# Kernel optimization log

Measured on AMD Instinct MI355X. Metric: run time of the kernel, lower is better.

## Reference

```python
import jax, jax.numpy as jnp
import numpy as np

C = 512        # in_ch = n_heads * d_embed
NH = 8         # heads
DH = C // NH   # head dim = 64
G = 32         # groups
EPS_GN = 1e-6
EPS_LN = 1e-5


def group_norm(x, gamma, beta):
    # x: (B, C, H, W)
    B, Cc, H, W = x.shape
    xg = x.reshape(B, G, Cc // G, H, W)
    mu = xg.mean(axis=(2, 3, 4), keepdims=True)
    var = xg.var(axis=(2, 3, 4), keepdims=True)
    xg = (xg - mu) * jax.lax.rsqrt(var + EPS_GN)
    x = xg.reshape(B, Cc, H, W)
    return x * gamma[None, :, None, None] + beta[None, :, None, None]


def layer_norm(x, gamma, beta):
    mu = x.mean(axis=-1, keepdims=True)
    var = x.var(axis=-1, keepdims=True)
    return (x - mu) * jax.lax.rsqrt(var + EPS_LN) * gamma + beta


def mhsa(x, w_qkv, w_out, b_out):
    # x: (B, S, C); w_qkv: (C, 3C); w_out: (C, C)
    B, S, Cc = x.shape
    qkv = x @ w_qkv                                   # (B, S, 3C)
    q, k, v = jnp.split(qkv, 3, axis=-1)
    q = q.reshape(B, S, NH, DH).transpose(0, 2, 1, 3)  # (B, H, S, D)
    k = k.reshape(B, S, NH, DH).transpose(0, 2, 1, 3)
    v = v.reshape(B, S, NH, DH).transpose(0, 2, 1, 3)
    scores = jnp.einsum('bhsd,bhtd->bhst', q, k) / jnp.sqrt(jnp.float32(DH))
    attn = jax.nn.softmax(scores, axis=-1)
    o = jnp.einsum('bhst,bhtd->bhsd', attn, v)         # (B, H, S, D)
    o = o.transpose(0, 2, 1, 3).reshape(B, S, Cc)
    return o @ w_out + b_out


def conv1x1(x, w, b):
    # x: (B, C, H, W); w: (Cout, Cin)
    return jnp.einsum('oc,bchw->bohw', w, x) + b[None, :, None, None]


def reference(x, gn_g, gn_b, w_cin, b_cin,
              ln1_g, ln1_b, qkv1, out1_w, out1_b,
              ln2_g, ln2_b, qkv2, out2_w, out2_b,
              ln3_g, ln3_b, g1_w, g1_b, g2_w, g2_b,
              w_cout, b_cout):
    residue_long = x
    h = group_norm(x, gn_g, gn_b)
    h = conv1x1(h, w_cin, b_cin)
    B, Cc, H, W = h.shape
    h = h.reshape(B, Cc, H * W).transpose(0, 2, 1)     # (B, S, C)

    r = h
    h = mhsa(layer_norm(h, ln1_g, ln1_b), qkv1, out1_w, out1_b) + r
    r = h
    h = mhsa(layer_norm(h, ln2_g, ln2_b), qkv2, out2_w, out2_b) + r
    r = h
    g = layer_norm(h, ln3_g, ln3_b) @ g1_w + g1_b      # (B, S, 8C)
    val, gate = jnp.split(g, 2, axis=-1)
    h = (val * jax.nn.gelu(gate, approximate=False)) @ g2_w + g2_b
    h = h + r

    h = h.transpose(0, 2, 1).reshape(B, Cc, H, W)
    return conv1x1(h, w_cout, b_cout) + residue_long


def setup_inputs() -> dict:
    key = jax.random.key(0)
    ks = jax.random.split(key, 16)
    s = lambda n: 1.0 / np.sqrt(n)
    return {
        'x': jax.random.normal(ks[0], (8, C, 32, 32), jnp.float32),
        'gn_g': jnp.ones((C,), jnp.float32),
        'gn_b': jnp.zeros((C,), jnp.float32),
        'w_cin': jax.random.normal(ks[1], (C, C), jnp.float32) * s(C),
        'b_cin': jnp.zeros((C,), jnp.float32),
        'ln1_g': jnp.ones((C,), jnp.float32),
        'ln1_b': jnp.zeros((C,), jnp.float32),
        'qkv1': jax.random.normal(ks[2], (C, 3 * C), jnp.float32) * s(C),
        'out1_w': jax.random.normal(ks[3], (C, C), jnp.float32) * s(C),
        'out1_b': jnp.zeros((C,), jnp.float32),
        'ln2_g': jnp.ones((C,), jnp.float32),
        'ln2_b': jnp.zeros((C,), jnp.float32),
        'qkv2': jax.random.normal(ks[4], (C, 3 * C), jnp.float32) * s(C),
        'out2_w': jax.random.normal(ks[5], (C, C), jnp.float32) * s(C),
        'out2_b': jnp.zeros((C,), jnp.float32),
        'ln3_g': jnp.ones((C,), jnp.float32),
        'ln3_b': jnp.zeros((C,), jnp.float32),
        'g1_w': jax.random.normal(ks[6], (C, 8 * C), jnp.float32) * s(C),
        'g1_b': jnp.zeros((8 * C,), jnp.float32),
        'g2_w': jax.random.normal(ks[7], (4 * C, C), jnp.float32) * s(4 * C),
        'g2_b': jnp.zeros((C,), jnp.float32),
        'w_cout': jax.random.normal(ks[8], (C, C), jnp.float32) * s(C),
        'b_cout': jnp.zeros((C,), jnp.float32),
    }
```

## Files before the change

kernel.cpp:

```cpp
#include <hip/hip_runtime.h>
#include <hip/hip_bf16.h>
#include <math.h>

typedef __hip_bfloat16 bf16;

typedef __bf16 bf16x8 __attribute__((ext_vector_type(8)));
typedef float f32x4 __attribute__((ext_vector_type(4)));
typedef short shortx8 __attribute__((ext_vector_type(8)));

__device__ __forceinline__ float b2f_us(unsigned short u) {
    unsigned int v = ((unsigned int)u) << 16;
    return __builtin_bit_cast(float, v);
}
__device__ __forceinline__ unsigned short f2b_us(float f) {
    return __builtin_bit_cast(unsigned short, __float2bfloat16(f));
}
__device__ __forceinline__ float4 ld4(const float* p) { return *(const float4*)p; }
__device__ __forceinline__ float4 ld4(const bf16* p) {
    ushort4 u = *(const ushort4*)p;
    return make_float4(b2f_us(u.x), b2f_us(u.y), b2f_us(u.z), b2f_us(u.w));
}
__device__ __forceinline__ bf16x8 ldfrag(const bf16* p) {
    return __builtin_bit_cast(bf16x8, *(const shortx8*)p);
}
__device__ __forceinline__ f32x4 mfma16(bf16x8 a, bf16x8 b, f32x4 c) {
    return __builtin_amdgcn_mfma_f32_16x16x32_bf16(a, b, c, 0, 0, 0);
}
__device__ __forceinline__ void gload16(const bf16* g, bf16* l) {
    __builtin_amdgcn_global_load_lds(
        (const __attribute__((address_space(1))) void*)g,
        (__attribute__((address_space(3))) void*)l, 16, 0, 0);
}

struct WJob { const float* src; bf16* dst; int R, C, tile0, trans; };
struct WJobs { WJob j[8]; };

__global__ __launch_bounds__(256) void wconv_all(WJobs jobs) {
    __shared__ float tl[32][33];
    int bid = blockIdx.x;
    int ji = 0;
#pragma unroll
    for (int i = 1; i < 8; ++i)
        if (bid >= jobs.j[i].tile0) ji = i;
    WJob jb = jobs.j[ji];
    int t = bid - jb.tile0;
    int tc = jb.C >> 5;
    int tr_ = t / tc, tcx = t - tr_ * tc;
    int r0 = tr_ * 32, c0 = tcx * 32;
    const int tx = threadIdx.x & 31, ty = threadIdx.x >> 5;
    if (jb.trans) {
#pragma unroll
        for (int i = 0; i < 4; ++i)
            tl[ty + i * 8][tx] = jb.src[(long)(r0 + ty + i * 8) * jb.C + c0 + tx];
        __syncthreads();
#pragma unroll
        for (int i = 0; i < 4; ++i)
            jb.dst[(long)(c0 + ty + i * 8) * jb.R + r0 + tx] =
                __float2bfloat16(tl[tx][ty + i * 8]);
    } else {
#pragma unroll
        for (int i = 0; i < 4; ++i) {
            long idx = (long)(r0 + ty + i * 8) * jb.C + c0 + tx;
            jb.dst[idx] = __float2bfloat16(jb.src[idx]);
        }
    }
}

__global__ __launch_bounds__(256) void gn_stats_k(const float* __restrict__ x,
                                                  float* __restrict__ stats) {
    int bg = blockIdx.x;
    long base = (long)bg * 16384;
    int tid = threadIdx.x;
    float s = 0.f, sq = 0.f;
    for (int it = 0; it < 16; ++it) {
        float4 v = *(const float4*)(x + base + (long)it * 1024 + tid * 4);
        s += v.x + v.y + v.z + v.w;
        sq += v.x * v.x + v.y * v.y + v.z * v.z + v.w * v.w;
    }
#pragma unroll
    for (int off = 32; off; off >>= 1) {
        s += __shfl_down(s, off);
        sq += __shfl_down(sq, off);
    }
    __shared__ float r0[4], r1[4];
    if ((tid & 63) == 0) { r0[tid >> 6] = s; r1[tid >> 6] = sq; }
    __syncthreads();
    if (tid == 0) {
        s = r0[0] + r0[1] + r0[2] + r0[3];
        sq = r1[0] + r1[1] + r1[2] + r1[3];
        float mu = s * (1.f / 16384.f);
        float var = sq * (1.f / 16384.f) - mu * mu;
        stats[bg] = mu;
        stats[256 + bg] = rsqrtf(var + 1e-6f);
    }
}

__global__ __launch_bounds__(256) void gnxt_k(const float* __restrict__ x,
                                              const float* __restrict__ stats,
                                              const float* __restrict__ gng,
                                              const float* __restrict__ gnb,
                                              bf16* __restrict__ xt) {
    const int b = blockIdx.z;
    const int c0 = blockIdx.y * 64, s0 = blockIdx.x * 64;
    __shared__ float t[64][65];
    const int tx = threadIdx.x & 15, ty = threadIdx.x >> 4;
#pragma unroll
    for (int i = 0; i < 4; ++i) {
        int c = c0 + ty + i * 16;
        float rs = stats[256 + b * 32 + (c >> 4)];
        float ga = gng[c] * rs;
        float be = gnb[c] - stats[b * 32 + (c >> 4)] * ga;
        float4 v = *(const float4*)(x + ((long)b * 512 + c) * 1024 + s0 + tx * 4);
        t[ty + i * 16][tx * 4 + 0] = v.x * ga + be;
        t[ty + i * 16][tx * 4 + 1] = v.y * ga + be;
        t[ty + i * 16][tx * 4 + 2] = v.z * ga + be;
        t[ty + i * 16][tx * 4 + 3] = v.w * ga + be;
    }
    __syncthreads();
#pragma unroll
    for (int i = 0; i < 4; ++i) {
        int s = s0 + ty + i * 16;
        ushort4 o;
        o.x = f2b_us(t[tx * 4 + 0][ty + i * 16]);
        o.y = f2b_us(t[tx * 4 + 1][ty + i * 16]);
        o.z = f2b_us(t[tx * 4 + 2][ty + i * 16]);
        o.w = f2b_us(t[tx * 4 + 3][ty + i * 16]);
        *(ushort4*)(xt + ((long)b * 1024 + s) * 512 + c0 + tx * 4) = o;
    }
}

__global__ __launch_bounds__(256) void ln_k(const bf16* __restrict__ in,
                                            const float* __restrict__ g,
                                            const float* __restrict__ bvec,
                                            bf16* __restrict__ out) {
    long row = blockIdx.x;
    const bf16* p = in + row * 512;
    int tid = threadIdx.x;
    float v0 = b2f_us(__builtin_bit_cast(unsigned short, p[tid]));
    float v1 = b2f_us(__builtin_bit_cast(unsigned short, p[tid + 256]));
    float s = v0 + v1, sq = v0 * v0 + v1 * v1;
#pragma unroll
    for (int off = 32; off; off >>= 1) {
        s += __shfl_down(s, off);
        sq += __shfl_down(sq, off);
    }
    __shared__ float r0[4], r1[4];
    if ((tid & 63) == 0) { r0[tid >> 6] = s; r1[tid >> 6] = sq; }
    __syncthreads();
    s = r0[0] + r0[1] + r0[2] + r0[3];
    sq = r1[0] + r1[1] + r1[2] + r1[3];
    float mu = s * (1.f / 512.f);
    float var = sq * (1.f / 512.f) - mu * mu;
    float rs = rsqrtf(var + 1e-5f);
    out[row * 512 + tid] = __float2bfloat16((v0 - mu) * rs * g[tid] + bvec[tid]);
    out[row * 512 + tid + 256] =
        __float2bfloat16((v1 - mu) * rs * g[tid + 256] + bvec[tid + 256]);
}

template <bool HASBIAS, bool HASRES>
__global__ __launch_bounds__(256, 2) void mm_k(
    const bf16* __restrict__ A, const bf16* __restrict__ Bw,
    const float* __restrict__ bias, const bf16* __restrict__ res,
    bf16* __restrict__ C, int lda, int ldb, int ldc, int NT) {
    __shared__ bf16 sA[8192];
    __shared__ bf16 sB[8192];
    const int lane = threadIdx.x & 63, wave = threadIdx.x >> 6;
    const int lr = lane & 15, lg = lane >> 4;
    const int wm = wave >> 1, wn = wave & 1;
    const int m0 = blockIdx.y * 128, n0 = blockIdx.x * 128;

    f32x4 acc[4][4];
#pragma unroll
    for (int i = 0; i < 4; ++i)
#pragma unroll
        for (int j = 0; j < 4; ++j) acc[i][j] = (f32x4){0.f, 0.f, 0.f, 0.f};

    for (int t = 0; t < NT; ++t) {
        const int k0 = t * 64;
#pragma unroll
        for (int q = 0; q < 4; ++q) {
            int st = wave * 4 + q;
            int kh = st >> 3, sm = st & 7;
            gload16(A + (long)(m0 + sm * 16 + lr) * lda + k0 + kh * 32 + lg * 8,
                    &sA[st << 9]);
            gload16(Bw + (long)(n0 + sm * 16 + lr) * ldb + k0 + kh * 32 + lg * 8,
                    &sB[st << 9]);
        }
        asm volatile("s_waitcnt vmcnt(0) lgkmcnt(0)" ::: "memory");
        __builtin_amdgcn_s_barrier();
#pragma unroll
        for (int kh = 0; kh < 2; ++kh) {
            bf16x8 af[4], bfr[4];
#pragma unroll
            for (int i = 0; i < 4; ++i)
                af[i] = ldfrag(&sA[((kh * 8 + wm * 4 + i) << 9) + lane * 8]);
#pragma unroll
            for (int j = 0; j < 4; ++j)
                bfr[j] = ldfrag(&sB[((kh * 8 + wn * 4 + j) << 9) + lane * 8]);
#pragma unroll
            for (int i = 0; i < 4; ++i)
#pragma unroll
                for (int j = 0; j < 4; ++j)
                    acc[i][j] = mfma16(af[i], bfr[j], acc[i][j]);
        }
        __builtin_amdgcn_s_barrier();
    }

#pragma unroll
    for (int i = 0; i < 4; ++i) {
        int row = m0 + wm * 64 + i * 16 + lg * 4;
#pragma unroll
        for (int j = 0; j < 4; ++j) {
            int col = n0 + wn * 64 + j * 16 + lr;
            float bv = HASBIAS ? bias[col] : 0.f;
#pragma unroll
            for (int r = 0; r < 4; ++r) {
                float v = acc[i][j][r] + bv;
                if (HASRES)
                    v += b2f_us(__builtin_bit_cast(unsigned short,
                             res[(long)(row + r) * ldc + col]));
                C[(long)(row + r) * ldc + col] = __float2bfloat16(v);
            }
        }
    }
}

__global__ __launch_bounds__(256, 2) void mm_geglu_k(
    const bf16* __restrict__ A, const bf16* __restrict__ Bv,
    const bf16* __restrict__ Bg, const float* __restrict__ bias,
    bf16* __restrict__ C, int NT) {
    __shared__ bf16 sA[8192];
    __shared__ bf16 sB[8192];
    const int lane = threadIdx.x & 63, wave = threadIdx.x >> 6;
    const int lr = lane & 15, lg = lane >> 4;
    const int wm = wave >> 1, wn = wave & 1;
    const int m0 = blockIdx.y * 128, n0 = blockIdx.x * 64;

    f32x4 accv[4][2], accg[4][2];
#pragma unroll
    for (int i = 0; i < 4; ++i)
#pragma unroll
        for (int j = 0; j < 2; ++j) {
            accv[i][j] = (f32x4){0.f, 0.f, 0.f, 0.f};
            accg[i][j] = (f32x4){0.f, 0.f, 0.f, 0.f};
        }

    for (int t = 0; t < NT; ++t) {
        const int k0 = t * 64;
#pragma unroll
        for (int q = 0; q < 4; ++q) {
            int st = wave * 4 + q;
            int kh = st >> 3, sm = st & 7;
            gload16(A + (long)(m0 + sm * 16 + lr) * 512 + k0 + kh * 32 + lg * 8,
                    &sA[st << 9]);
            const bf16* bsrc = (sm < 4) ? Bv : Bg;
            int sn = sm & 3;
            gload16(bsrc + (long)(n0 + sn * 16 + lr) * 512 + k0 + kh * 32 + lg * 8,
                    &sB[st << 9]);
        }
        asm volatile("s_waitcnt vmcnt(0) lgkmcnt(0)" ::: "memory");
        __builtin_amdgcn_s_barrier();
#pragma unroll
        for (int kh = 0; kh < 2; ++kh) {
            bf16x8 af[4], bv_[2], bg_[2];
#pragma unroll
            for (int i = 0; i < 4; ++i)
                af[i] = ldfrag(&sA[((kh * 8 + wm * 4 + i) << 9) + lane * 8]);
#pragma unroll
            for (int j = 0; j < 2; ++j) {
                bv_[j] = ldfrag(&sB[((kh * 8 + wn * 2 + j) << 9) + lane * 8]);
                bg_[j] = ldfrag(&sB[((kh * 8 + 4 + wn * 2 + j) << 9) + lane * 8]);
            }
#pragma unroll
            for (int i = 0; i < 4; ++i)
#pragma unroll
                for (int j = 0; j < 2; ++j) {
                    accv[i][j] = mfma16(af[i], bv_[j], accv[i][j]);
                    accg[i][j] = mfma16(af[i], bg_[j], accg[i][j]);
                }
        }
        __builtin_amdgcn_s_barrier();
    }

#pragma unroll
    for (int i = 0; i < 4; ++i) {
        int row = m0 + wm * 64 + i * 16 + lg * 4;
#pragma unroll
        for (int j = 0; j < 2; ++j) {
            int col = n0 + (wn * 2 + j) * 16 + lr;
            float bv = bias[col], bg2 = bias[2048 + col];
#pragma unroll
            for (int r = 0; r < 4; ++r) {
                float v = accv[i][j][r] + bv;
                float g = accg[i][j][r] + bg2;
                float gl = 0.5f * g * (1.f + erff(g * 0.70710678118654752f));
                C[(long)(row + r) * 2048 + col] = __float2bfloat16(v * gl);
            }
        }
    }
}

__global__ __launch_bounds__(256) void vtrans_k(const bf16* __restrict__ qkv,
                                                bf16* __restrict__ vt) {
    const int bh = blockIdx.y;
    const int b = bh >> 3, h = bh & 7;
    const int s0 = blockIdx.x * 64;
    __shared__ bf16 tl[64][72];
    const int sl = threadIdx.x >> 2, q = threadIdx.x & 3;
    const bf16* src = qkv + ((long)b * 1024 + s0 + sl) * 1536 + 1024 + h * 64;
    *(shortx8*)&tl[sl][q * 8] = *(const shortx8*)(src + q * 8);
    *(shortx8*)&tl[sl][32 + q * 8] = *(const shortx8*)(src + 32 + q * 8);
    __syncthreads();
    const int dl = threadIdx.x >> 2;
    bf16* dst = vt + ((long)bh * 64 + dl) * 1024 + s0;
#pragma unroll
    for (int c = 0; c < 2; ++c) {
        int sb = c * 32 + q * 8;
        shortx8 o;
#pragma unroll
        for (int i = 0; i < 8; ++i)
            o[i] = __builtin_bit_cast(short, tl[sb + i][dl]);
        *(shortx8*)(dst + sb) = o;
    }
}

__global__ __launch_bounds__(256) void attn_mfma_k(const bf16* __restrict__ qkv,
                                                   const bf16* __restrict__ vt,
                                                   bf16* __restrict__ o) {
    const int wave = threadIdx.x >> 6, lane = threadIdx.x & 63;
    const int lr = lane & 15, lg = lane >> 4;
    const int h = blockIdx.y, b = blockIdx.z;
    const int q0 = blockIdx.x * 128 + wave * 32;
    __shared__ bf16 sKV[8192];
    __shared__ bf16 plds[4][16][72];
    bf16* pl = &plds[wave][0][0];
    const bf16* qbase = qkv + (long)b * 1024 * 1536 + h * 64;
    const bf16* kbase = qbase + 512;
    const bf16* vbase = vt + ((long)(b * 8 + h) * 64) * 1024;

    bf16x8 qf[2][2];
#pragma unroll
    for (int s = 0; s < 2; ++s) {
        const bf16* qp = qbase + (long)(q0 + s * 16 + lr) * 1536 + lg * 8;
#pragma unroll
        for (int c = 0; c < 2; ++c) {
            shortx8 raw = *(const shortx8*)(qp + c * 32);
            shortx8 sc;
#pragma unroll
            for (int j = 0; j < 8; ++j)
                sc[j] = __builtin_bit_cast(short,
                    f2b_us(b2f_us((unsigned short)raw[j]) * 0.125f));
            qf[s][c] = __builtin_bit_cast(bf16x8, sc);
        }
    }

    f32x4 of[2][4];
    float mrow[2][4], lrow[2][4];
#pragma unroll
    for (int s = 0; s < 2; ++s)
#pragma unroll
        for (int r = 0; r < 4; ++r) {
            of[s][r] = (f32x4){0.f, 0.f, 0.f, 0.f};
            mrow[s][r] = -1e30f;
            lrow[s][r] = 0.f;
        }

    for (int t = 0; t < 16; ++t) {
        const int kv0 = t * 64;
#pragma unroll
        for (int q = 0; q < 4; ++q) {
            int st = wave * 4 + q;
            const bf16* src;
            if (st < 8)
                src = kbase + (long)(kv0 + (st >> 1) * 16 + lr) * 1536 +
                      (st & 1) * 32 + lg * 8;
            else
                src = vbase + (long)(((st - 8) >> 1) * 16 + lr) * 1024 + kv0 +
                      (st & 1) * 32 + lg * 8;
            gload16(src, &sKV[st << 9]);
        }
        asm volatile("s_waitcnt vmcnt(0) lgkmcnt(0)" ::: "memory");
        __builtin_amdgcn_s_barrier();

        f32x4 sf[2][4];
        __builtin_amdgcn_s_setprio(1);
#pragma unroll
        for (int kt = 0; kt < 4; ++kt) {
            bf16x8 k0f = ldfrag(&sKV[(kt * 2) * 512 + lane * 8]);
            bf16x8 k1f = ldfrag(&sKV[(kt * 2 + 1) * 512 + lane * 8]);
#pragma unroll
            for (int s = 0; s < 2; ++s) {
                f32x4 z = {0.f, 0.f, 0.f, 0.f};
                z = mfma16(qf[s][0], k0f, z);
                z = mfma16(qf[s][1], k1f, z);
                sf[s][kt] = z;
            }
        }
        __builtin_amdgcn_s_setprio(0);

        bf16x8 pa[2][2];
#pragma unroll
        for (int s = 0; s < 2; ++s) {
            float mt[4];
#pragma unroll
            for (int r = 0; r < 4; ++r)
                mt[r] = fmaxf(fmaxf(sf[s][0][r], sf[s][1][r]),
                              fmaxf(sf[s][2][r], sf[s][3][r]));
#pragma unroll
            for (int m = 1; m < 16; m <<= 1)
#pragma unroll
                for (int r = 0; r < 4; ++r)
                    mt[r] = fmaxf(mt[r], __shfl_xor(mt[r], m));
            float al[4];
#pragma unroll
            for (int r = 0; r < 4; ++r) {
                float mn = fmaxf(mrow[s][r], mt[r]);
                al[r] = __expf(mrow[s][r] - mn);
                mrow[s][r] = mn;
            }
            float psum[4] = {0.f, 0.f, 0.f, 0.f};
#pragma unroll
            for (int kt = 0; kt < 4; ++kt)
#pragma unroll
                for (int r = 0; r < 4; ++r) {
                    float p = __expf(sf[s][kt][r] - mrow[s][r]);
                    psum[r] += p;
                    pl[(lg * 4 + r) * 72 + kt * 16 + lr] = __float2bfloat16(p);
                }
#pragma unroll
            for (int m = 1; m < 16; m <<= 1)
#pragma unroll
                for (int r = 0; r < 4; ++r)
                    psum[r] += __shfl_xor(psum[r], m);
#pragma unroll
            for (int r = 0; r < 4; ++r)
                lrow[s][r] = lrow[s][r] * al[r] + psum[r];
#pragma unroll
            for (int dt = 0; dt < 4; ++dt)
#pragma unroll
                for (int r = 0; r < 4; ++r) of[s][dt][r] *= al[r];
            pa[s][0] = ldfrag(pl + lr * 72 + lg * 8);
            pa[s][1] = ldfrag(pl + lr * 72 + 32 + lg * 8);
        }
        __builtin_amdgcn_s_setprio(1);
#pragma unroll
        for (int dt = 0; dt < 4; ++dt) {
            bf16x8 v0f = ldfrag(&sKV[(8 + dt * 2) * 512 + lane * 8]);
            bf16x8 v1f = ldfrag(&sKV[(8 + dt * 2 + 1) * 512 + lane * 8]);
#pragma unroll
            for (int s = 0; s < 2; ++s) {
                of[s][dt] = mfma16(pa[s][0], v0f, of[s][dt]);
                of[s][dt] = mfma16(pa[s][1], v1f, of[s][dt]);
            }
        }
        __builtin_amdgcn_s_setprio(0);
        __builtin_amdgcn_s_barrier();
    }

#pragma unroll
    for (int s = 0; s < 2; ++s) {
        bf16* op = o + ((long)b * 1024 + q0 + s * 16 + lg * 4) * 512 + h * 64 + lr;
#pragma unroll
        for (int r = 0; r < 4; ++r) {
            float inv = 1.f / lrow[s][r];
#pragma unroll
            for (int dt = 0; dt < 4; ++dt)
                op[(long)r * 512 + dt * 16] = __float2bfloat16(of[s][dt][r] * inv);
        }
    }
}

__global__ __launch_bounds__(256) void outepi_k(const bf16* __restrict__ tmp,
                                                const float* __restrict__ bcout,
                                                const float* __restrict__ x,
                                                float* __restrict__ out) {
    const int b = blockIdx.z;
    const int o0 = blockIdx.y * 64, s0 = blockIdx.x * 64;
    __shared__ float t[64][65];
    const int tx = threadIdx.x & 15, ty = threadIdx.x >> 4;
#pragma unroll
    for (int i = 0; i < 4; ++i) {
        int s = s0 + ty + i * 16;
        float4 v = ld4(tmp + ((long)b * 1024 + s) * 512 + o0 + tx * 4);
        t[ty + i * 16][tx * 4 + 0] = v.x;
        t[ty + i * 16][tx * 4 + 1] = v.y;
        t[ty + i * 16][tx * 4 + 2] = v.z;
        t[ty + i * 16][tx * 4 + 3] = v.w;
    }
    __syncthreads();
#pragma unroll
    for (int i = 0; i < 4; ++i) {
        int o = o0 + ty + i * 16;
        long idx = ((long)b * 512 + o) * 1024 + s0 + tx * 4;
        float4 xr = *(const float4*)(x + idx);
        float bc = bcout[o];
        float4 w;
        w.x = t[tx * 4 + 0][ty + i * 16] + bc + xr.x;
        w.y = t[tx * 4 + 1][ty + i * 16] + bc + xr.y;
        w.z = t[tx * 4 + 2][ty + i * 16] + bc + xr.z;
        w.w = t[tx * 4 + 3][ty + i * 16] + bc + xr.w;
        *(float4*)(out + idx) = w;
    }
}

extern "C" void kernel_launch(void* const* d_in, const int* in_sizes, int n_in,
                              void* d_out, int out_size, void* d_ws, size_t ws_size,
                              hipStream_t stream) {
    const float* x = (const float*)d_in[0];
    const float* gn_g = (const float*)d_in[1];
    const float* gn_b = (const float*)d_in[2];
    const float* w_cin = (const float*)d_in[3];
    const float* b_cin = (const float*)d_in[4];
    const float* ln1_g = (const float*)d_in[5];
    const float* ln1_b = (const float*)d_in[6];
    const float* qkv1w = (const float*)d_in[7];
    const float* out1_w = (const float*)d_in[8];
    const float* out1_b = (const float*)d_in[9];
    const float* ln2_g = (const float*)d_in[10];
    const float* ln2_b = (const float*)d_in[11];
    const float* qkv2w = (const float*)d_in[12];
    const float* out2_w = (const float*)d_in[13];
    const float* out2_b = (const float*)d_in[14];
    const float* ln3_g = (const float*)d_in[15];
    const float* ln3_b = (const float*)d_in[16];
    const float* g1_w = (const float*)d_in[17];
    const float* g1_b = (const float*)d_in[18];
    const float* g2_w = (const float*)d_in[19];
    const float* g2_b = (const float*)d_in[20];
    const float* w_cout = (const float*)d_in[21];
    const float* b_cout = (const float*)d_in[22];
    float* out = (float*)d_out;

    char* ws = (char*)d_ws;
    float* stats = (float*)ws;
    bf16* wq1 = (bf16*)(ws + 4096);
    bf16* wo1 = wq1 + 1536 * 512;
    bf16* wq2 = wo1 + 512 * 512;
    bf16* wo2 = wq2 + 1536 * 512;
    bf16* wg1 = wo2 + 512 * 512;
    bf16* wg2 = wg1 + 4096 * 512;
    bf16* wci = wg2 + 512 * 2048;
    bf16* wco = wci + 512 * 512;
    bf16* h = wco + 512 * 512;
    bf16* h2 = h + (size_t)8192 * 512;
    bf16* lnb = h2 + (size_t)8192 * 512;
    bf16* qkv = lnb + (size_t)8192 * 512;
    bf16* obuf = qkv + (size_t)8192 * 1536;
    bf16* gg = qkv;
    bf16* vt = lnb;

    WJobs jobs;
    jobs.j[0] = {qkv1w, wq1, 512, 1536, 0, 1};
    jobs.j[1] = {out1_w, wo1, 512, 512, 768, 1};
    jobs.j[2] = {qkv2w, wq2, 512, 1536, 1024, 1};
    jobs.j[3] = {out2_w, wo2, 512, 512, 1792, 1};
    jobs.j[4] = {g1_w, wg1, 512, 4096, 2048, 1};
    jobs.j[5] = {g2_w, wg2, 2048, 512, 4096, 1};
    jobs.j[6] = {w_cin, wci, 512, 512, 5120, 0};
    jobs.j[7] = {w_cout, wco, 512, 512, 5376, 0};
    wconv_all<<<5632, 256, 0, stream>>>(jobs);

    gn_stats_k<<<256, 256, 0, stream>>>(x, stats);
    gnxt_k<<<dim3(16, 8, 8), 256, 0, stream>>>(x, stats, gn_g, gn_b, lnb);
    mm_k<true, false><<<dim3(4, 64), 256, 0, stream>>>(
        lnb, wci, b_cin, nullptr, h, 512, 512, 512, 8);

    ln_k<<<8192, 256, 0, stream>>>(h, ln1_g, ln1_b, lnb);
    mm_k<false, false><<<dim3(12, 64), 256, 0, stream>>>(
        lnb, wq1, nullptr, nullptr, qkv, 512, 512, 1536, 8);
    vtrans_k<<<dim3(16, 64), 256, 0, stream>>>(qkv, vt);
    attn_mfma_k<<<dim3(8, 8, 8), 256, 0, stream>>>(qkv, vt, obuf);
    mm_k<true, true><<<dim3(4, 64), 256, 0, stream>>>(
        obuf, wo1, out1_b, h, h2, 512, 512, 512, 8);

    ln_k<<<8192, 256, 0, stream>>>(h2, ln2_g, ln2_b, lnb);
    mm_k<false, false><<<dim3(12, 64), 256, 0, stream>>>(
        lnb, wq2, nullptr, nullptr, qkv, 512, 512, 1536, 8);
    vtrans_k<<<dim3(16, 64), 256, 0, stream>>>(qkv, vt);
    attn_mfma_k<<<dim3(8, 8, 8), 256, 0, stream>>>(qkv, vt, obuf);
    mm_k<true, true><<<dim3(4, 64), 256, 0, stream>>>(
        obuf, wo2, out2_b, h2, h, 512, 512, 512, 8);

    ln_k<<<8192, 256, 0, stream>>>(h, ln3_g, ln3_b, lnb);
    mm_geglu_k<<<dim3(32, 64), 256, 0, stream>>>(
        lnb, wg1, wg1 + (size_t)2048 * 512, g1_b, gg, 8);
    mm_k<true, true><<<dim3(4, 64), 256, 0, stream>>>(
        gg, wg2, g2_b, h, h2, 2048, 2048, 512, 32);

    mm_k<false, false><<<dim3(4, 64), 256, 0, stream>>>(
        h2, wco, nullptr, nullptr, lnb, 512, 512, 512, 8);
    outepi_k<<<dim3(16, 8, 8), 256, 0, stream>>>(lnb, b_cout, x, out);
}
```

Measured before the change: 436.2 us.

## Narrow GEMM tiles for N=512, fuse V transpose into QKV GEMM, lazy softmax rescale

Templates the GEMM on tile width, so the N=512 GEMMs use 128x64 tiles with twice the blocks, and raises launch bounds to 3 blocks per CU. The QKV GEMM epilogue writes V directly in transposed layout, which removes the separate vtrans kernel and its extra pass over memory. Attention now loads 128 keys per barrier instead of 64, and skips the online-softmax rescale unless the running max grows by more than 8. Each of these changes costs something: smaller tiles reuse less data, LDS usage grows, and the lazy rescale bounds exponents only by e^8 before normalisation.

```diff
diff --git a/kernel.cpp b/kernel.cpp
--- a/kernel.cpp
+++ b/kernel.cpp
@@ -157,23 +157,25 @@
         __float2bfloat16((v1 - mu) * rs * g[tid + 256] + bvec[tid + 256]);
 }
 
-template <bool HASBIAS, bool HASRES>
-__global__ __launch_bounds__(256, 2) void mm_k(
+template <bool HASBIAS, bool HASRES, int BN, bool VSPLIT>
+__global__ __launch_bounds__(256, 3) void mm_k(
     const bf16* __restrict__ A, const bf16* __restrict__ Bw,
     const float* __restrict__ bias, const bf16* __restrict__ res,
-    bf16* __restrict__ C, int lda, int ldb, int ldc, int NT) {
+    bf16* __restrict__ C, bf16* __restrict__ vtout,
+    int lda, int ldb, int ldc, int NT) {
+    constexpr int NJ = BN / 64 * 2;
     __shared__ bf16 sA[8192];
-    __shared__ bf16 sB[8192];
+    __shared__ bf16 sB[BN == 128 ? 8192 : 4096];
     const int lane = threadIdx.x & 63, wave = threadIdx.x >> 6;
     const int lr = lane & 15, lg = lane >> 4;
     const int wm = wave >> 1, wn = wave & 1;
-    const int m0 = blockIdx.y * 128, n0 = blockIdx.x * 128;
-
-    f32x4 acc[4][4];
+    const int m0 = blockIdx.y * 128, n0 = blockIdx.x * BN;
+
+    f32x4 acc[4][NJ];
 #pragma unroll
     for (int i = 0; i < 4; ++i)
 #pragma unroll
-        for (int j = 0; j < 4; ++j) acc[i][j] = (f32x4){0.f, 0.f, 0.f, 0.f};
+        for (int j = 0; j < NJ; ++j) acc[i][j] = (f32x4){0.f, 0.f, 0.f, 0.f};
 
     for (int t = 0; t < NT; ++t) {
         const int k0 = t * 64;
@@ -183,35 +185,72 @@
             int kh = st >> 3, sm = st & 7;
             gload16(A + (long)(m0 + sm * 16 + lr) * lda + k0 + kh * 32 + lg * 8,
                     &sA[st << 9]);
-            gload16(Bw + (long)(n0 + sm * 16 + lr) * ldb + k0 + kh * 32 + lg * 8,
-                    &sB[st << 9]);
+        }
+        if (BN == 128) {
+#pragma unroll
+            for (int q = 0; q < 4; ++q) {
+                int st = wave * 4 + q;
+                int kh = st >> 3, sn = st & 7;
+                gload16(Bw + (long)(n0 + sn * 16 + lr) * ldb + k0 + kh * 32 + lg * 8,
+                        &sB[st << 9]);
+            }
+        } else {
+#pragma unroll
+            for (int q = 0; q < 2; ++q) {
+                int bs = wave * 2 + q;
+                int kh = bs >> 2, sn = bs & 3;
+                gload16(Bw + (long)(n0 + sn * 16 + lr) * ldb + k0 + kh * 32 + lg * 8,
+                        &sB[bs << 9]);
+            }
         }
         asm volatile("s_waitcnt vmcnt(0) lgkmcnt(0)" ::: "memory");
         __builtin_amdgcn_s_barrier();
 #pragma unroll
         for (int kh = 0; kh < 2; ++kh) {
-            bf16x8 af[4], bfr[4];
+            bf16x8 af[4], bfr[NJ];
 #pragma unroll
             for (int i = 0; i < 4; ++i)
                 af[i] = ldfrag(&sA[((kh * 8 + wm * 4 + i) << 9) + lane * 8]);
 #pragma unroll
-            for (int j = 0; j < 4; ++j)
-                bfr[j] = ldfrag(&sB[((kh * 8 + wn * 4 + j) << 9) + lane * 8]);
+            for (int j = 0; j < NJ; ++j) {
+                int bs = BN == 128 ? (kh * 8 + wn * 4 + j) : (kh * 4 + wn * 2 + j);
+                bfr[j] = ldfrag(&sB[(bs << 9) + lane * 8]);
+            }
 #pragma unroll
             for (int i = 0; i < 4; ++i)
 #pragma unroll
-                for (int j = 0; j < 4; ++j)
+                for (int j = 0; j < NJ; ++j)
                     acc[i][j] = mfma16(af[i], bfr[j], acc[i][j]);
         }
         __builtin_amdgcn_s_barrier();
     }
 
+    if (VSPLIT && n0 >= 1024) {
+#pragma unroll
+        for (int i = 0; i < 4; ++i) {
+            int row = m0 + wm * 64 + i * 16 + lg * 4;
+            int bb = row >> 10, ss = row & 1023;
+#pragma unroll
+            for (int j = 0; j < NJ; ++j) {
+                int col = n0 + wn * (BN / 2) + j * 16 + lr;
+                int v = col - 1024;
+                int hh = v >> 6, dd = v & 63;
+                ushort4 o4;
+                o4.x = f2b_us(acc[i][j][0]);
+                o4.y = f2b_us(acc[i][j][1]);
+                o4.z = f2b_us(acc[i][j][2]);
+                o4.w = f2b_us(acc[i][j][3]);
+                *(ushort4*)(vtout + ((long)(bb * 8 + hh) * 64 + dd) * 1024 + ss) = o4;
+            }
+        }
+        return;
+    }
 #pragma unroll
     for (int i = 0; i < 4; ++i) {
         int row = m0 + wm * 64 + i * 16 + lg * 4;
 #pragma unroll
-        for (int j = 0; j < 4; ++j) {
-            int col = n0 + wn * 64 + j * 16 + lr;
+        for (int j = 0; j < NJ; ++j) {
+            int col = n0 + wn * (BN / 2) + j * 16 + lr;
             float bv = HASBIAS ? bias[col] : 0.f;
 #pragma unroll
             for (int r = 0; r < 4; ++r) {
@@ -300,30 +339,6 @@
     }
 }
 
-__global__ __launch_bounds__(256) void vtrans_k(const bf16* __restrict__ qkv,
-                                                bf16* __restrict__ vt) {
-    const int bh = blockIdx.y;
-    const int b = bh >> 3, h = bh & 7;
-    const int s0 = blockIdx.x * 64;
-    __shared__ bf16 tl[64][72];
-    const int sl = threadIdx.x >> 2, q = threadIdx.x & 3;
-    const bf16* src = qkv + ((long)b * 1024 + s0 + sl) * 1536 + 1024 + h * 64;
-    *(shortx8*)&tl[sl][q * 8] = *(const shortx8*)(src + q * 8);
-    *(shortx8*)&tl[sl][32 + q * 8] = *(const shortx8*)(src + 32 + q * 8);
-    __syncthreads();
-    const int dl = threadIdx.x >> 2;
-    bf16* dst = vt + ((long)bh * 64 + dl) * 1024 + s0;
-#pragma unroll
-    for (int c = 0; c < 2; ++c) {
-        int sb = c * 32 + q * 8;
-        shortx8 o;
-#pragma unroll
-        for (int i = 0; i < 8; ++i)
-            o[i] = __builtin_bit_cast(short, tl[sb + i][dl]);
-        *(shortx8*)(dst + sb) = o;
-    }
-}
-
 __global__ __launch_bounds__(256) void attn_mfma_k(const bf16* __restrict__ qkv,
                                                    const bf16* __restrict__ vt,
                                                    bf16* __restrict__ o) {
@@ -331,7 +346,7 @@
     const int lr = lane & 15, lg = lane >> 4;
     const int h = blockIdx.y, b = blockIdx.z;
     const int q0 = blockIdx.x * 128 + wave * 32;
-    __shared__ bf16 sKV[8192];
+    __shared__ bf16 sKV[16384];
     __shared__ bf16 plds[4][16][72];
     bf16* pl = &plds[wave][0][0];
     const bf16* qbase = qkv + (long)b * 1024 * 1536 + h * 64;
@@ -365,29 +380,13 @@
             lrow[s][r] = 0.f;
         }
 
-    for (int t = 0; t < 16; ++t) {
-        const int kv0 = t * 64;
-#pragma unroll
-        for (int q = 0; q < 4; ++q) {
-            int st = wave * 4 + q;
-            const bf16* src;
-            if (st < 8)
-                src = kbase + (long)(kv0 + (st >> 1) * 16 + lr) * 1536 +
-                      (st & 1) * 32 + lg * 8;
-            else
-                src = vbase + (long)(((st - 8) >> 1) * 16 + lr) * 1024 + kv0 +
-                      (st & 1) * 32 + lg * 8;
-            gload16(src, &sKV[st << 9]);
-        }
-        asm volatile("s_waitcnt vmcnt(0) lgkmcnt(0)" ::: "memory");
-        __builtin_amdgcn_s_barrier();
-
+    auto computeKV = [&](const bf16* base) {
         f32x4 sf[2][4];
         __builtin_amdgcn_s_setprio(1);
 #pragma unroll
         for (int kt = 0; kt < 4; ++kt) {
-            bf16x8 k0f = ldfrag(&sKV[(kt * 2) * 512 + lane * 8]);
-            bf16x8 k1f = ldfrag(&sKV[(kt * 2 + 1) * 512 + lane * 8]);
+            bf16x8 k0f = ldfrag(base + (kt * 2) * 512 + lane * 8);
+            bf16x8 k1f = ldfrag(base + (kt * 2 + 1) * 512 + lane * 8);
 #pragma unroll
             for (int s = 0; s < 2; ++s) {
                 f32x4 z = {0.f, 0.f, 0.f, 0.f};
@@ -411,12 +410,19 @@
 #pragma unroll
                 for (int r = 0; r < 4; ++r)
                     mt[r] = fmaxf(mt[r], __shfl_xor(mt[r], m));
-            float al[4];
-#pragma unroll
-            for (int r = 0; r < 4; ++r) {
-                float mn = fmaxf(mrow[s][r], mt[r]);
-                al[r] = __expf(mrow[s][r] - mn);
-                mrow[s][r] = mn;
+            float need = mt[0] - mrow[s][0];
+#pragma unroll
+            for (int r = 1; r < 4; ++r) need = fmaxf(need, mt[r] - mrow[s][r]);
+            if (!__all(need <= 8.f)) {
+#pragma unroll
+                for (int r = 0; r < 4; ++r) {
+                    float mn = fmaxf(mrow[s][r], mt[r]);
+                    float al = __expf(mrow[s][r] - mn);
+                    mrow[s][r] = mn;
+                    lrow[s][r] *= al;
+#pragma unroll
+                    for (int dt = 0; dt < 4; ++dt) of[s][dt][r] *= al;
+                }
             }
             float psum[4] = {0.f, 0.f, 0.f, 0.f};
 #pragma unroll
@@ -433,20 +439,15 @@
                 for (int r = 0; r < 4; ++r)
                     psum[r] += __shfl_xor(psum[r], m);
 #pragma unroll
-            for (int r = 0; r < 4; ++r)
-                lrow[s][r] = lrow[s][r] * al[r] + psum[r];
-#pragma unroll
-            for (int dt = 0; dt < 4; ++dt)
-#pragma unroll
-                for (int r = 0; r < 4; ++r) of[s][dt][r] *= al[r];
+            for (int r = 0; r < 4; ++r) lrow[s][r] += psum[r];
             pa[s][0] = ldfrag(pl + lr * 72 + lg * 8);
             pa[s][1] = ldfrag(pl + lr * 72 + 32 + lg * 8);
         }
         __builtin_amdgcn_s_setprio(1);
 #pragma unroll
         for (int dt = 0; dt < 4; ++dt) {
-            bf16x8 v0f = ldfrag(&sKV[(8 + dt * 2) * 512 + lane * 8]);
-            bf16x8 v1f = ldfrag(&sKV[(8 + dt * 2 + 1) * 512 + lane * 8]);
+            bf16x8 v0f = ldfrag(base + (8 + dt * 2) * 512 + lane * 8);
+            bf16x8 v1f = ldfrag(base + (8 + dt * 2 + 1) * 512 + lane * 8);
 #pragma unroll
             for (int s = 0; s < 2; ++s) {
                 of[s][dt] = mfma16(pa[s][0], v0f, of[s][dt]);
@@ -454,6 +455,30 @@
             }
         }
         __builtin_amdgcn_s_setprio(0);
+    };
+
+    for (int t = 0; t < 8; ++t) {
+        const int kv0 = t * 128;
+#pragma unroll
+        for (int q = 0; q < 8; ++q) {
+            int st = wave * 8 + q;
+            int chunk = st >> 4, r = st & 15;
+            int kvb = kv0 + chunk * 64;
+            const bf16* src;
+            if (r < 8)
+                src = kbase + (long)(kvb + (r >> 1) * 16 + lr) * 1536 +
+                      (r & 1) * 32 + lg * 8;
+            else {
+                int vs = r - 8;
+                src = vbase + (long)((vs >> 1) * 16 + lr) * 1024 + kvb +
+                      (vs & 1) * 32 + lg * 8;
+            }
+            gload16(src, &sKV[st << 9]);
+        }
+        asm volatile("s_waitcnt vmcnt(0) lgkmcnt(0)" ::: "memory");
+        __builtin_amdgcn_s_barrier();
+        computeKV(&sKV[0]);
+        computeKV(&sKV[8192]);
         __builtin_amdgcn_s_barrier();
     }
 
@@ -547,7 +572,7 @@
     bf16* qkv = lnb + (size_t)8192 * 512;
     bf16* obuf = qkv + (size_t)8192 * 1536;
     bf16* gg = qkv;
-    bf16* vt = lnb;
+    bf16* vt = obuf;
 
     WJobs jobs;
     jobs.j[0] = {qkv1w, wq1, 512, 1536, 0, 1};
@@ -562,32 +587,30 @@
 
     gn_stats_k<<<256, 256, 0, stream>>>(x, stats);
     gnxt_k<<<dim3(16, 8, 8), 256, 0, stream>>>(x, stats, gn_g, gn_b, lnb);
-    mm_k<true, false><<<dim3(4, 64), 256, 0, stream>>>(
-        lnb, wci, b_cin, nullptr, h, 512, 512, 512, 8);
+    mm_k<true, false, 64, false><<<dim3(8, 64), 256, 0, stream>>>(
+        lnb, wci, b_cin, nullptr, h, nullptr, 512, 512, 512, 8);
 
     ln_k<<<8192, 256, 0, stream>>>(h, ln1_g, ln1_b, lnb);
-    mm_k<false, false><<<dim3(12, 64), 256, 0, stream>>>(
-        lnb, wq1, nullptr, nullptr, qkv, 512, 512, 1536, 8);
-    vtrans_k<<<dim3(16, 64), 256, 0, stream>>>(qkv, vt);
-    attn_mfma_k<<<dim3(8, 8, 8), 256, 0, stream>>>(qkv, vt, obuf);
-    mm_k<true, true><<<dim3(4, 64), 256, 0, stream>>>(
-        obuf, wo1, out1_b, h, h2, 512, 512, 512, 8);
+    mm_k<false, false, 128, true><<<dim3(12, 64), 256, 0, stream>>>(
+        lnb, wq1, nullptr, nullptr, qkv, vt, 512, 512, 1536, 8);
+    attn_mfma_k<<<dim3(8, 8, 8), 256, 0, stream>>>(qkv, vt, lnb);
+    mm_k<true, true, 64, false><<<dim3(8, 64), 256, 0, stream>>>(
+        lnb, wo1, out1_b, h, h2, nullptr, 512, 512, 512, 8);
 
     ln_k<<<8192, 256, 0, stream>>>(h2, ln2_g, ln2_b, lnb);
-    mm_k<false, false><<<dim3(12, 64), 256, 0, stream>>>(
-        lnb, wq2, nullptr, nullptr, qkv, 512, 512, 1536, 8);
-    vtrans_k<<<dim3(16, 64), 256, 0, stream>>>(qkv, vt);
-    attn_mfma_k<<<dim3(8, 8, 8), 256, 0, stream>>>(qkv, vt, obuf);
-    mm_k<true, true><<<dim3(4, 64), 256, 0, stream>>>(
-        obuf, wo2, out2_b, h2, h, 512, 512, 512, 8);
+    mm_k<false, false, 128, true><<<dim3(12, 64), 256, 0, stream>>>(
+        lnb, wq2, nullptr, nullptr, qkv, vt, 512, 512, 1536, 8);
+    attn_mfma_k<<<dim3(8, 8, 8), 256, 0, stream>>>(qkv, vt, lnb);
+    mm_k<true, true, 64, false><<<dim3(8, 64), 256, 0, stream>>>(
+        lnb, wo2, out2_b, h2, h, nullptr, 512, 512, 512, 8);
 
     ln_k<<<8192, 256, 0, stream>>>(h, ln3_g, ln3_b, lnb);
     mm_geglu_k<<<dim3(32, 64), 256, 0, stream>>>(
         lnb, wg1, wg1 + (size_t)2048 * 512, g1_b, gg, 8);
-    mm_k<true, true><<<dim3(4, 64), 256, 0, stream>>>(
-        gg, wg2, g2_b, h, h2, 2048, 2048, 512, 32);
-
-    mm_k<false, false><<<dim3(4, 64), 256, 0, stream>>>(
-        h2, wco, nullptr, nullptr, lnb, 512, 512, 512, 8);
+    mm_k<true, true, 64, false><<<dim3(8, 64), 256, 0, stream>>>(
+        gg, wg2, g2_b, h, h2, nullptr, 2048, 2048, 512, 32);
+
+    mm_k<false, false, 64, false><<<dim3(8, 64), 256, 0, stream>>>(
+        h2, wco, nullptr, nullptr, lnb, nullptr, 512, 512, 512, 8);
     outepi_k<<<dim3(16, 8, 8), 256, 0, stream>>>(lnb, b_cout, x, out);
 }
```

Result: faster. 407.3 us (-6.6%).
